# Performance work log

Measured on AMD Instinct MI355X. Metric: run time of the kernel, lower is better.

The kernel has to match this reference:

```python
import jax, jax.numpy as jnp
import numpy as np

B, T, C, H, DH = 4, 2048, 1024, 16, 64  # batch, seq (block_size), n_embd, heads, head_size


def setup_inputs() -> dict:
    key = jax.random.key(0)
    ks = jax.random.split(key, 6)
    x = jax.random.normal(ks[0], (B, T, C), dtype=jnp.float32)
    init = 0.02
    Wq = jax.random.normal(ks[1], (H, C, DH), dtype=jnp.float32) * init
    Wk = jax.random.normal(ks[2], (H, C, DH), dtype=jnp.float32) * init
    Wv = jax.random.normal(ks[3], (H, C, DH), dtype=jnp.float32) * init
    Wp = jax.random.normal(ks[4], (H * DH, C), dtype=jnp.float32) * init
    bp = jnp.zeros((C,), dtype=jnp.float32)
    return {"x": x, "Wq": Wq, "Wk": Wk, "Wv": Wv, "Wp": Wp, "bp": bp}


def reference(x, Wq, Wk, Wv, Wp, bp):
    Bb, Tt, Cc = x.shape
    # per-head projections, vectorized over heads (original loops in Python)
    q = jnp.einsum('btc,hcd->bhtd', x, Wq)
    k = jnp.einsum('btc,hcd->bhtd', x, Wk)
    v = jnp.einsum('btc,hcd->bhtd', x, Wv)
    # NOTE: original scales by rsqrt(C) where C is the INPUT embed dim, not head_size
    scale = 1.0 / jnp.sqrt(jnp.asarray(Cc, dtype=x.dtype))
    wei = jnp.einsum('bhtd,bhsd->bhts', q, k) * scale  # [B,H,T,T]
    causal = jnp.tril(jnp.ones((Tt, Tt), dtype=bool))
    wei = jnp.where(causal, wei, -jnp.inf)
    wei = jax.nn.softmax(wei, axis=-1)
    out = jnp.einsum('bhts,bhsd->bhtd', wei, v)  # [B,H,T,DH]
    # concat heads along feature axis (head h -> slice h*DH:(h+1)*DH)
    out = out.transpose(0, 2, 1, 3).reshape(Bb, Tt, -1)  # [B,T,H*DH]
    out = out @ Wp + bp  # output projection to n_embd
    return out
```

## Files before the change

kernel.cpp:

```cpp
#include <hip/hip_runtime.h>

#define TSEQ 2048
#define CDIM 1024
#define NH 16
#define DH 64
#define NB 4

typedef __bf16 bf16x8 __attribute__((ext_vector_type(8)));
typedef float f32x4 __attribute__((ext_vector_type(4)));

#define QSCALE 0.04508422f

static __device__ __forceinline__ ushort f2bf(float f) {
  unsigned u = __float_as_uint(f);
  unsigned r = u + 0x7fffu + ((u >> 16) & 1u);
  return (ushort)(r >> 16);
}

static __device__ __forceinline__ uint cvtpk(float lo, float hi) {
  uint r;
  asm("v_cvt_pk_bf16_f32 %0, %1, %2" : "=v"(r) : "v"(lo), "v"(hi));
  return r;
}

static __device__ __forceinline__ void gload_lds16(const void* g, void* ldsbase) {
  __builtin_amdgcn_global_load_lds((const __attribute__((address_space(1))) void*)g,
                                   (__attribute__((address_space(3))) void*)ldsbase,
                                   16, 0, 0);
}

__global__ void cvt_x_kernel(const float4* __restrict__ src, ushort4* __restrict__ dst, int n4) {
  int i = blockIdx.x * blockDim.x + threadIdx.x;
  if (i >= n4) return;
  float4 f = src[i];
  ushort4 o;
  o.x = f2bf(f.x); o.y = f2bf(f.y); o.z = f2bf(f.z); o.w = f2bf(f.w);
  dst[i] = o;
}

__global__ void transpose_cvt_kernel(const float* __restrict__ src, ushort* __restrict__ dst,
                                     int R, int Cc) {
  __shared__ float tile[32][33];
  const float* s = src + (size_t)blockIdx.z * R * Cc;
  ushort* d = dst + (size_t)blockIdx.z * R * Cc;
  int c0 = blockIdx.x * 32, r0 = blockIdx.y * 32;
  int tx = threadIdx.x, ty = threadIdx.y;
  for (int i = ty; i < 32; i += 8) {
    int r = r0 + i, c = c0 + tx;
    tile[i][tx] = (r < R && c < Cc) ? s[(size_t)r * Cc + c] : 0.f;
  }
  __syncthreads();
  for (int i = ty; i < 32; i += 8) {
    int c = c0 + i, r = r0 + tx;
    if (c < Cc && r < R) d[(size_t)c * R + r] = f2bf(tile[tx][i]);
  }
}

template <int MODE>
__global__ __launch_bounds__(256) void gemm_kernel(
    const ushort* __restrict__ A, const ushort* __restrict__ Bt,
    const float* __restrict__ bp, float* __restrict__ fout,
    ushort* __restrict__ qb, ushort* __restrict__ kb, ushort* __restrict__ vTb) {
  __shared__ ushort lds[16384];
  const int tid = threadIdx.x, w = tid >> 6, l = tid & 63;
  const int nwg = gridDim.x;
  const int bid = blockIdx.x;
  const int wgid = (bid & 7) * (nwg >> 3) + (bid >> 3);
  const int NT = (MODE == 0) ? 24 : 8;
  const int nt = wgid % NT, mt = wgid / NT;
  const int wr = w >> 1, wc = w & 1;
  const int srow = l >> 3;
  const int scol = (((l & 7) ^ srow) << 3);
  char* ldsb = (char*)lds;

  f32x4 acc[4][4] = {};

  for (int k0 = 0; k0 < CDIM; k0 += 64) {
#pragma unroll
    for (int i = 0; i < 8; ++i) {
      int ch = w * 8 + i;
      if (ch < 16) {
        gload_lds16(A + ((size_t)mt * 128 + ch * 8 + srow) * CDIM + k0 + scol, ldsb + ch * 1024);
      } else {
        gload_lds16(Bt + ((size_t)nt * 128 + (ch - 16) * 8 + srow) * CDIM + k0 + scol,
                    ldsb + ch * 1024);
      }
    }
    __syncthreads();
#pragma unroll
    for (int ks = 0; ks < 2; ++ks) {
      bf16x8 af[4];
#pragma unroll
      for (int fm = 0; fm < 4; ++fm) {
        int row = wr * 64 + fm * 16 + (l & 15);
        int cb = (ks * 64 + 16 * (l >> 4)) ^ ((row & 7) << 4);
        af[fm] = *(const bf16x8*)(ldsb + row * 128 + cb);
      }
#pragma unroll
      for (int fn = 0; fn < 4; ++fn) {
        int n = wc * 64 + fn * 16 + (l & 15);
        int cb = (ks * 64 + 16 * (l >> 4)) ^ ((n & 7) << 4);
        bf16x8 bfr = *(const bf16x8*)(ldsb + 16384 + n * 128 + cb);
#pragma unroll
        for (int fm = 0; fm < 4; ++fm)
          acc[fm][fn] = __builtin_amdgcn_mfma_f32_16x16x32_bf16(af[fm], bfr, acc[fm][fn], 0, 0, 0);
      }
    }
    __syncthreads();
  }

#pragma unroll
  for (int fm = 0; fm < 4; ++fm) {
#pragma unroll
    for (int fn = 0; fn < 4; ++fn) {
      const int gr0 = mt * 128 + wr * 64 + fm * 16 + (l >> 4) * 4;
      const int gc = nt * 128 + wc * 64 + fn * 16 + (l & 15);
      if (MODE == 1) {
        float bias = bp[gc];
#pragma unroll
        for (int r = 0; r < 4; ++r)
          fout[(size_t)(gr0 + r) * CDIM + gc] = acc[fm][fn][r] + bias;
      } else {
        const int sel = gc >> 10, h = (gc >> 6) & 15, d = gc & 63;
        const int bh = (gr0 >> 11) * NH + h, tl = gr0 & 2047;
        if (sel == 2) {
          ushort4 pk;
          pk.x = f2bf(acc[fm][fn][0]); pk.y = f2bf(acc[fm][fn][1]);
          pk.z = f2bf(acc[fm][fn][2]); pk.w = f2bf(acc[fm][fn][3]);
          *(ushort4*)(vTb + ((size_t)bh * DH + d) * TSEQ + tl) = pk;
        } else if (sel == 0) {
#pragma unroll
          for (int r = 0; r < 4; ++r)
            qb[((size_t)bh * TSEQ + tl + r) * DH + d] = f2bf(acc[fm][fn][r] * QSCALE);
        } else {
#pragma unroll
          for (int r = 0; r < 4; ++r)
            kb[((size_t)bh * TSEQ + tl + r) * DH + d] = f2bf(acc[fm][fn][r]);
        }
      }
    }
  }
}

__global__ __launch_bounds__(256, 3) void attn_kernel(
    const ushort* __restrict__ qb, const ushort* __restrict__ kb,
    const ushort* __restrict__ vTb, ushort* __restrict__ aob) {
  __shared__ ushort lds[16384];
  char* ldsb = (char*)lds;
  const int tid = threadIdx.x, w = tid >> 6, l = tid & 63;
  const int id = blockIdx.x;
  const int bh = (id & 7) * 8 + ((id >> 3) & 7);
  const int qt = 15 - (id >> 6);
  const int q0 = qt * 128;
  const int nt = 2 * (qt + 1);
  const int b = bh >> 4, h = bh & 15;
  const int g = l >> 4, q = l & 15;
  const int srow = l >> 3;
  const int scol = (((l & 7) ^ srow) << 3);
  const int adrA = ((l & 16) << 1 | q) << 2;
  const int adrB = adrA + 64;
  const bool hi32 = (l & 32) != 0;

  bf16x8 qf[2][2];
#pragma unroll
  for (int qs = 0; qs < 2; ++qs) {
    const ushort* qrow = qb + ((size_t)bh * TSEQ + q0 + w * 32 + qs * 16 + q) * DH;
    qf[qs][0] = *(const bf16x8*)(qrow + 8 * g);
    qf[qs][1] = *(const bf16x8*)(qrow + 32 + 8 * g);
  }

  float m[2] = {-1e30f, -1e30f}, lsum[2] = {0.f, 0.f};
  f32x4 o[4][2] = {};

#pragma unroll
  for (int i = 0; i < 4; ++i) {
    int ch = w * 4 + i;
    if (ch < 8)
      gload_lds16(kb + ((size_t)bh * TSEQ + ch * 8 + srow) * DH + scol, ldsb + ch * 1024);
    else {
      int d = (ch - 8) * 8 + srow;
      gload_lds16(vTb + ((size_t)bh * DH + d) * TSEQ + scol, ldsb + 16384 + (ch - 8) * 1024);
    }
  }

#pragma unroll 1
  for (int j = 0; j < nt; ++j) {
    __syncthreads();
    const int cbuf = j & 1;
    if (j + 1 < nt) {
      const int kvn = (j + 1) * 64, nb = (j + 1) & 1;
#pragma unroll
      for (int i = 0; i < 4; ++i) {
        int ch = w * 4 + i;
        if (ch < 8)
          gload_lds16(kb + ((size_t)bh * TSEQ + kvn + ch * 8 + srow) * DH + scol,
                      ldsb + nb * 8192 + ch * 1024);
        else {
          int d = (ch - 8) * 8 + srow;
          gload_lds16(vTb + ((size_t)bh * DH + d) * TSEQ + kvn + scol,
                      ldsb + 16384 + nb * 8192 + (ch - 8) * 1024);
        }
      }
    }
    char* Kb = ldsb + cbuf * 8192;
    char* Vb = ldsb + 16384 + cbuf * 8192;

    f32x4 s[4][2] = {};
    __builtin_amdgcn_s_setprio(1);
#pragma unroll
    for (int ks = 0; ks < 2; ++ks)
#pragma unroll
      for (int fn = 0; fn < 4; ++fn) {
        int n = fn * 16 + q;
        int cbb = (ks * 64 + 16 * g) ^ ((n & 7) << 4);
        bf16x8 kf = *(const bf16x8*)(Kb + n * 128 + cbb);
        s[fn][0] = __builtin_amdgcn_mfma_f32_16x16x32_bf16(kf, qf[0][ks], s[fn][0], 0, 0, 0);
        s[fn][1] = __builtin_amdgcn_mfma_f32_16x16x32_bf16(kf, qf[1][ks], s[fn][1], 0, 0, 0);
      }
    __builtin_amdgcn_s_setprio(0);

    if (j >= nt - 2) {
#pragma unroll
      for (int qs = 0; qs < 2; ++qs) {
        int rowloc = q0 + w * 32 + qs * 16 + q - j * 64;
#pragma unroll
        for (int fn = 0; fn < 4; ++fn)
#pragma unroll
          for (int r = 0; r < 4; ++r)
            if (fn * 16 + 4 * g + r > rowloc) s[fn][qs][r] = -1e30f;
      }
    }

    float rm[2];
#pragma unroll
    for (int qs = 0; qs < 2; ++qs) {
      float v = -1e30f;
#pragma unroll
      for (int fn = 0; fn < 4; ++fn)
        v = fmaxf(v, fmaxf(fmaxf(s[fn][qs][0], s[fn][qs][1]), fmaxf(s[fn][qs][2], s[fn][qs][3])));
      v = fmaxf(v, __shfl_xor(v, 16));
      v = fmaxf(v, __shfl_xor(v, 32));
      rm[qs] = v;
    }

    if (__any(fmaxf(rm[0] - m[0], rm[1] - m[1]) > 8.f)) {
      float fc[2];
#pragma unroll
      for (int qs = 0; qs < 2; ++qs) {
        float mn = fmaxf(m[qs], rm[qs]);
        fc[qs] = __builtin_amdgcn_exp2f(m[qs] - mn);
        m[qs] = mn; lsum[qs] *= fc[qs];
      }
#pragma unroll
      for (int r = 0; r < 4; ++r) {
        float f0 = __shfl(fc[0], (l & 0x30) | (4 * g + r), 64);
        float f1 = __shfl(fc[1], (l & 0x30) | (4 * g + r), 64);
#pragma unroll
        for (int fn = 0; fn < 4; ++fn) { o[fn][0][r] *= f0; o[fn][1][r] *= f1; }
      }
    }

    uint D[2][4][2];
#pragma unroll
    for (int qs = 0; qs < 2; ++qs) {
      float rs = 0.f;
#pragma unroll
      for (int fn = 0; fn < 4; ++fn) {
        float p0 = __builtin_amdgcn_exp2f(s[fn][qs][0] - m[qs]);
        float p1 = __builtin_amdgcn_exp2f(s[fn][qs][1] - m[qs]);
        float p2 = __builtin_amdgcn_exp2f(s[fn][qs][2] - m[qs]);
        float p3 = __builtin_amdgcn_exp2f(s[fn][qs][3] - m[qs]);
        rs += (p0 + p1) + (p2 + p3);
        D[qs][fn][0] = cvtpk(p0, p1);
        D[qs][fn][1] = cvtpk(p2, p3);
      }
      rs += __shfl_xor(rs, 16);
      rs += __shfl_xor(rs, 32);
      lsum[qs] += rs;
    }

#pragma unroll
    for (int ksg = 0; ksg < 2; ++ksg) {
      union { uint u[4]; bf16x8 v; } P[2];
#pragma unroll
      for (int qs = 0; qs < 2; ++qs) {
        uint t0a = __builtin_amdgcn_ds_bpermute(adrA, (int)D[qs][2 * ksg][0]);
        uint t0b = __builtin_amdgcn_ds_bpermute(adrA, (int)D[qs][2 * ksg + 1][0]);
        uint t1a = __builtin_amdgcn_ds_bpermute(adrA, (int)D[qs][2 * ksg][1]);
        uint t1b = __builtin_amdgcn_ds_bpermute(adrA, (int)D[qs][2 * ksg + 1][1]);
        uint t2a = __builtin_amdgcn_ds_bpermute(adrB, (int)D[qs][2 * ksg][0]);
        uint t2b = __builtin_amdgcn_ds_bpermute(adrB, (int)D[qs][2 * ksg + 1][0]);
        uint t3a = __builtin_amdgcn_ds_bpermute(adrB, (int)D[qs][2 * ksg][1]);
        uint t3b = __builtin_amdgcn_ds_bpermute(adrB, (int)D[qs][2 * ksg + 1][1]);
        P[qs].u[0] = hi32 ? t0b : t0a;
        P[qs].u[1] = hi32 ? t1b : t1a;
        P[qs].u[2] = hi32 ? t2b : t2a;
        P[qs].u[3] = hi32 ? t3b : t3a;
      }
      __builtin_amdgcn_s_setprio(1);
#pragma unroll
      for (int fn = 0; fn < 4; ++fn) {
        int n = fn * 16 + q;
        int cbb = (ksg * 64 + 16 * g) ^ ((n & 7) << 4);
        bf16x8 vf = *(const bf16x8*)(Vb + n * 128 + cbb);
        o[fn][0] = __builtin_amdgcn_mfma_f32_16x16x32_bf16(P[0].v, vf, o[fn][0], 0, 0, 0);
        o[fn][1] = __builtin_amdgcn_mfma_f32_16x16x32_bf16(P[1].v, vf, o[fn][1], 0, 0, 0);
      }
      __builtin_amdgcn_s_setprio(0);
    }
  }

#pragma unroll
  for (int qs = 0; qs < 2; ++qs) {
    float inv = 1.f / lsum[qs];
#pragma unroll
    for (int r = 0; r < 4; ++r) {
      float invq = __shfl(inv, (l & 0x30) | (4 * g + r), 64);
      int t = q0 + w * 32 + qs * 16 + 4 * g + r;
#pragma unroll
      for (int fn = 0; fn < 4; ++fn) {
        int d = fn * 16 + q;
        aob[((size_t)b * TSEQ + t) * (NH * DH) + h * DH + d] = f2bf(o[fn][qs][r] * invq);
      }
    }
  }
}

extern "C" void kernel_launch(void* const* d_in, const int* in_sizes, int n_in,
                              void* d_out, int out_size, void* d_ws, size_t ws_size,
                              hipStream_t stream) {
  (void)in_sizes; (void)n_in; (void)out_size; (void)ws_size;
  const float* x  = (const float*)d_in[0];
  const float* Wq = (const float*)d_in[1];
  const float* Wk = (const float*)d_in[2];
  const float* Wv = (const float*)d_in[3];
  const float* Wp = (const float*)d_in[4];
  const float* bp = (const float*)d_in[5];
  float* out = (float*)d_out;
  char* ws = (char*)d_ws;

  ushort* xb  = (ushort*)(ws);
  ushort* wall = (ushort*)(ws + (16ull << 20));
  ushort* wqT = wall;
  ushort* wkT = wall + (1ull << 20);
  ushort* wvT = wall + (2ull << 20);
  ushort* wpT = (ushort*)(ws + (22ull << 20));
  ushort* qb  = (ushort*)(ws + (24ull << 20));
  ushort* kb  = (ushort*)(ws + (40ull << 20));
  ushort* vTb = (ushort*)(ws + (56ull << 20));
  ushort* aob = (ushort*)(ws + (72ull << 20));

  cvt_x_kernel<<<(NB * TSEQ * CDIM / 4 + 255) / 256, 256, 0, stream>>>(
      (const float4*)x, (ushort4*)xb, NB * TSEQ * CDIM / 4);
  transpose_cvt_kernel<<<dim3(2, 32, 16), dim3(32, 8), 0, stream>>>(Wq, wqT, CDIM, DH);
  transpose_cvt_kernel<<<dim3(2, 32, 16), dim3(32, 8), 0, stream>>>(Wk, wkT, CDIM, DH);
  transpose_cvt_kernel<<<dim3(2, 32, 16), dim3(32, 8), 0, stream>>>(Wv, wvT, CDIM, DH);
  transpose_cvt_kernel<<<dim3(32, 32, 1), dim3(32, 8), 0, stream>>>(Wp, wpT, CDIM, CDIM);

  gemm_kernel<0><<<dim3(64 * 24), 256, 0, stream>>>(xb, wall, nullptr, nullptr, qb, kb, vTb);
  attn_kernel<<<dim3(1024), 256, 0, stream>>>(qb, kb, vTb, aob);
  gemm_kernel<1><<<dim3(64 * 8), 256, 0, stream>>>(aob, wpT, bp, out, nullptr, nullptr, nullptr);
}
```

Baseline: 185.0 us.

## Double-buffer GEMM LDS tiles and merge weight transpose launches

The GEMM kernel now double-buffers its LDS tiles. It prefetches the next K-slice into the alternate buffer while the current slice runs through MFMA, and it drops one barrier per iteration. This is meant to hide global-to-LDS load latency behind compute. The cost is twice the LDS per workgroup (64KB), which may lower occupancy. Separately, the four weight transpose/convert launches are merged into one kernel to cut launch overhead.

```diff
diff --git a/kernel.cpp b/kernel.cpp
--- a/kernel.cpp
+++ b/kernel.cpp
@@ -38,22 +38,26 @@
   dst[i] = o;
 }
 
-__global__ void transpose_cvt_kernel(const float* __restrict__ src, ushort* __restrict__ dst,
-                                     int R, int Cc) {
+__global__ void transpose_cvt_all(const float* __restrict__ Wq, const float* __restrict__ Wk,
+                                  const float* __restrict__ Wv, const float* __restrict__ Wp,
+                                  ushort* __restrict__ wall, ushort* __restrict__ wpT) {
   __shared__ float tile[32][33];
-  const float* s = src + (size_t)blockIdx.z * R * Cc;
-  ushort* d = dst + (size_t)blockIdx.z * R * Cc;
-  int c0 = blockIdx.x * 32, r0 = blockIdx.y * 32;
-  int tx = threadIdx.x, ty = threadIdx.y;
-  for (int i = ty; i < 32; i += 8) {
-    int r = r0 + i, c = c0 + tx;
-    tile[i][tx] = (r < R && c < Cc) ? s[(size_t)r * Cc + c] : 0.f;
-  }
+  const int z = blockIdx.z;
+  const float* s; ushort* d; int Cc, c0, r0;
+  if (z < 3) {
+    const int head = blockIdx.x >> 1;
+    s = (z == 0 ? Wq : z == 1 ? Wk : Wv) + (size_t)head * CDIM * DH;
+    d = wall + ((size_t)z << 20) + (size_t)head * CDIM * DH;
+    Cc = DH; c0 = (blockIdx.x & 1) * 32; r0 = blockIdx.y * 32;
+  } else {
+    s = Wp; d = wpT; Cc = CDIM; c0 = blockIdx.x * 32; r0 = blockIdx.y * 32;
+  }
+  const int tx = threadIdx.x, ty = threadIdx.y;
+  for (int i = ty; i < 32; i += 8)
+    tile[i][tx] = s[(size_t)(r0 + i) * Cc + c0 + tx];
   __syncthreads();
-  for (int i = ty; i < 32; i += 8) {
-    int c = c0 + i, r = r0 + tx;
-    if (c < Cc && r < R) d[(size_t)c * R + r] = f2bf(tile[tx][i]);
-  }
+  for (int i = ty; i < 32; i += 8)
+    d[(size_t)(c0 + i) * CDIM + r0 + tx] = f2bf(tile[tx][i]);
 }
 
 template <int MODE>
@@ -61,7 +65,7 @@
     const ushort* __restrict__ A, const ushort* __restrict__ Bt,
     const float* __restrict__ bp, float* __restrict__ fout,
     ushort* __restrict__ qb, ushort* __restrict__ kb, ushort* __restrict__ vTb) {
-  __shared__ ushort lds[16384];
+  __shared__ ushort lds[32768];
   const int tid = threadIdx.x, w = tid >> 6, l = tid & 63;
   const int nwg = gridDim.x;
   const int bid = blockIdx.x;
@@ -75,18 +79,32 @@
 
   f32x4 acc[4][4] = {};
 
+  const ushort* Arow = A + ((size_t)mt * 128) * CDIM;
+  const ushort* Brow = Bt + ((size_t)nt * 128) * CDIM;
+
+#pragma unroll
+  for (int i = 0; i < 8; ++i) {
+    int ch = w * 8 + i;
+    const ushort* src = (ch < 16) ? Arow + (size_t)(ch * 8 + srow) * CDIM + scol
+                                  : Brow + (size_t)((ch - 16) * 8 + srow) * CDIM + scol;
+    gload_lds16(src, ldsb + ch * 1024);
+  }
+
   for (int k0 = 0; k0 < CDIM; k0 += 64) {
-#pragma unroll
-    for (int i = 0; i < 8; ++i) {
-      int ch = w * 8 + i;
-      if (ch < 16) {
-        gload_lds16(A + ((size_t)mt * 128 + ch * 8 + srow) * CDIM + k0 + scol, ldsb + ch * 1024);
-      } else {
-        gload_lds16(Bt + ((size_t)nt * 128 + (ch - 16) * 8 + srow) * CDIM + k0 + scol,
-                    ldsb + ch * 1024);
-      }
-    }
+    const int bsel = (k0 >> 6) & 1;
+    char* base = ldsb + bsel * 32768;
     __syncthreads();
+    if (k0 + 64 < CDIM) {
+      char* nbase = ldsb + (bsel ^ 1) * 32768;
+#pragma unroll
+      for (int i = 0; i < 8; ++i) {
+        int ch = w * 8 + i;
+        const ushort* src = (ch < 16)
+            ? Arow + (size_t)(ch * 8 + srow) * CDIM + k0 + 64 + scol
+            : Brow + (size_t)((ch - 16) * 8 + srow) * CDIM + k0 + 64 + scol;
+        gload_lds16(src, nbase + ch * 1024);
+      }
+    }
 #pragma unroll
     for (int ks = 0; ks < 2; ++ks) {
       bf16x8 af[4];
@@ -94,19 +112,18 @@
       for (int fm = 0; fm < 4; ++fm) {
         int row = wr * 64 + fm * 16 + (l & 15);
         int cb = (ks * 64 + 16 * (l >> 4)) ^ ((row & 7) << 4);
-        af[fm] = *(const bf16x8*)(ldsb + row * 128 + cb);
+        af[fm] = *(const bf16x8*)(base + row * 128 + cb);
       }
 #pragma unroll
       for (int fn = 0; fn < 4; ++fn) {
         int n = wc * 64 + fn * 16 + (l & 15);
         int cb = (ks * 64 + 16 * (l >> 4)) ^ ((n & 7) << 4);
-        bf16x8 bfr = *(const bf16x8*)(ldsb + 16384 + n * 128 + cb);
+        bf16x8 bfr = *(const bf16x8*)(base + 16384 + n * 128 + cb);
 #pragma unroll
         for (int fm = 0; fm < 4; ++fm)
           acc[fm][fn] = __builtin_amdgcn_mfma_f32_16x16x32_bf16(af[fm], bfr, acc[fm][fn], 0, 0, 0);
       }
     }
-    __syncthreads();
   }
 
 #pragma unroll
@@ -341,9 +358,6 @@
 
   ushort* xb  = (ushort*)(ws);
   ushort* wall = (ushort*)(ws + (16ull << 20));
-  ushort* wqT = wall;
-  ushort* wkT = wall + (1ull << 20);
-  ushort* wvT = wall + (2ull << 20);
   ushort* wpT = (ushort*)(ws + (22ull << 20));
   ushort* qb  = (ushort*)(ws + (24ull << 20));
   ushort* kb  = (ushort*)(ws + (40ull << 20));
@@ -352,10 +366,7 @@
 
   cvt_x_kernel<<<(NB * TSEQ * CDIM / 4 + 255) / 256, 256, 0, stream>>>(
       (const float4*)x, (ushort4*)xb, NB * TSEQ * CDIM / 4);
-  transpose_cvt_kernel<<<dim3(2, 32, 16), dim3(32, 8), 0, stream>>>(Wq, wqT, CDIM, DH);
-  transpose_cvt_kernel<<<dim3(2, 32, 16), dim3(32, 8), 0, stream>>>(Wk, wkT, CDIM, DH);
-  transpose_cvt_kernel<<<dim3(2, 32, 16), dim3(32, 8), 0, stream>>>(Wv, wvT, CDIM, DH);
-  transpose_cvt_kernel<<<dim3(32, 32, 1), dim3(32, 8), 0, stream>>>(Wp, wpT, CDIM, CDIM);
+  transpose_cvt_all<<<dim3(32, 32, 4), dim3(32, 8), 0, stream>>>(Wq, Wk, Wv, Wp, wall, wpT);
 
   gemm_kernel<0><<<dim3(64 * 24), 256, 0, stream>>>(xb, wall, nullptr, nullptr, qb, kb, vTb);
   attn_kernel<<<dim3(1024), 256, 0, stream>>>(qb, kb, vTb, aob);
```

New measurement: 181.1 us. 1.02x faster.
